# Performance work log

Measured on AMD Instinct MI355X. Metric: run time of the kernel, lower is better.

Reference implementation:

```python
import jax, jax.numpy as jnp
import numpy as np

B = 262144      # Monte Carlo samples (batch)
DH = 128        # d_hidden
DM = 4          # concatenated input feature dim (two one-hot spins)


def _glorot(key, shape):
    fan_in, fan_out = shape[0], shape[1]
    lim = jnp.sqrt(6.0 / (fan_in + fan_out)).astype(jnp.float32)
    return jax.random.uniform(key, shape, jnp.float32, -lim, lim)


def setup_inputs() -> dict:
    key = jax.random.key(0)
    ks = jax.random.split(key, 10)
    inputs = jax.random.normal(ks[0], (B, DM), jnp.float32)
    h1 = jax.random.normal(ks[1], (B, DH), jnp.float32)
    h2 = jax.random.normal(ks[2], (B, DH), jnp.float32)
    U1 = _glorot(ks[3], (DH, DH))
    U2 = _glorot(ks[4], (DH, DH))
    # flax GRUCell params: input kernels (with bias), hidden kernels
    # (r,z: no bias; n: bias). Packed as [ir|iz|in] and [hr|hz].
    Wi = _glorot(ks[5], (DM, 3 * DH))
    bi = jnp.zeros((3 * DH,), jnp.float32)
    Whrz = _glorot(ks[6], (DH, 2 * DH))
    Whn = _glorot(ks[7], (DH, DH))
    bhn = jnp.zeros((DH,), jnp.float32)
    return {"inputs": inputs, "h1": h1, "h2": h2, "U1": U1, "U2": U2,
            "Wi": Wi, "bi": bi, "Whrz": Whrz, "Whn": Whn, "bhn": bhn}


def reference(inputs, h1, h2, U1, U2, Wi, bi, Whrz, Whn, bhn):
    # Fuse the two neighbor hidden states: h = h1 @ U1 + h2 @ U2
    h = h1 @ U1 + h2 @ U2                      # [B, DH]
    # flax GRUCell(carry=h, inputs=x):
    i_proj = inputs @ Wi + bi                  # [B, 3*DH]
    ir, iz, i_n = jnp.split(i_proj, 3, axis=-1)
    hrz = h @ Whrz                             # [B, 2*DH] (no bias in flax)
    hr, hz = jnp.split(hrz, 2, axis=-1)
    r = jax.nn.sigmoid(ir + hr)
    z = jax.nn.sigmoid(iz + hz)
    n = jnp.tanh(i_n + r * (h @ Whn + bhn))
    new_h = (1.0 - z) * n + z * h
    return (new_h, new_h)
```

## Files before the change

### kernel.cpp

```cpp
#include <hip/hip_runtime.h>

using bf8 = __attribute__((ext_vector_type(8))) short;
using bf4 = __attribute__((ext_vector_type(4))) short;
using f4  = __attribute__((ext_vector_type(4))) float;
using u16 = unsigned short;

#define NROWS 262144

#define FLAG_B   0
#define PU_B     128
#define PW2_B    (PU_B + 65536)
#define PWI_B    (PW2_B + 98304)
#define BI_B     (PWI_B + 6144)
#define BHN_B    (BI_B + 1536)

#define PACK_ITEMS 83968

static __device__ __forceinline__ float bf2f(u16 u) {
    unsigned v = ((unsigned)u) << 16;
    return __builtin_bit_cast(float, v);
}
static __device__ __forceinline__ u16 f2bf(float f) {
    unsigned x = __builtin_bit_cast(unsigned, f);
    x = x + 0x7fffu + ((x >> 16) & 1u);
    return (u16)(x >> 16);
}

template<bool FP32>
static __device__ __forceinline__ u16 ldw(const void* p, int i) {
    if constexpr (FP32) return f2bf(((const float*)p)[i]);
    else                return ((const u16*)p)[i];
}
template<bool FP32>
static __device__ __forceinline__ float ldf(const void* p, int i) {
    if constexpr (FP32) return ((const float*)p)[i];
    else                return bf2f(((const u16*)p)[i]);
}
template<bool FP32>
static __device__ __forceinline__ bf8 ld8(const void* base, int idx) {
    if constexpr (!FP32) {
        return *(const bf8*)((const u16*)base + idx);
    } else {
        const float* f = (const float*)base + idx;
        f4 u = *(const f4*)f;
        f4 v = *(const f4*)(f + 4);
        bf8 r;
        r[0]=(short)f2bf(u[0]); r[1]=(short)f2bf(u[1]); r[2]=(short)f2bf(u[2]); r[3]=(short)f2bf(u[3]);
        r[4]=(short)f2bf(v[0]); r[5]=(short)f2bf(v[1]); r[6]=(short)f2bf(v[2]); r[7]=(short)f2bf(v[3]);
        return r;
    }
}
template<bool FP32>
static __device__ __forceinline__ void st8(void* base, int idx, bf8 v) {
    if constexpr (!FP32) {
        *(bf8*)((u16*)base + idx) = v;
    } else {
        float* f = (float*)base + idx;
        f4 a, b;
        a[0]=bf2f((u16)v[0]); a[1]=bf2f((u16)v[1]); a[2]=bf2f((u16)v[2]); a[3]=bf2f((u16)v[3]);
        b[0]=bf2f((u16)v[4]); b[1]=bf2f((u16)v[5]); b[2]=bf2f((u16)v[6]); b[3]=bf2f((u16)v[7]);
        *(f4*)f = a; *(f4*)(f + 4) = b;
    }
}

__global__ void detect_mode(const u16* __restrict__ h1u, int* __restrict__ flag) {
    if (threadIdx.x == 0 && blockIdx.x == 0) {
        int huge = 0;
#pragma unroll 8
        for (int i = 0; i < 256; ++i) {
            u16 v = h1u[i * 2];
            huge += (((v >> 7) & 0xFF) >= 0xC0);
        }
        *flag = (huge > 0) ? 1 : 0;
    }
}

template<bool FP32>
__global__ void prep_pack(const void* __restrict__ U1, const void* __restrict__ U2,
                          const void* __restrict__ Whrz, const void* __restrict__ Whn,
                          const void* __restrict__ Wi, const void* __restrict__ bi,
                          const void* __restrict__ bhn, char* __restrict__ ws,
                          const int* __restrict__ flag)
{
    if ((*flag != 0) != FP32) return;
    int e = blockIdx.x * 256 + threadIdx.x;
    if (e >= PACK_ITEMS) return;
    u16*   pU   = (u16*)(ws + PU_B);
    u16*   pW2  = (u16*)(ws + PW2_B);
    float* wiF  = (float*)(ws + PWI_B);
    float* biF  = (float*)(ws + BI_B);
    float* bhnF = (float*)(ws + BHN_B);
    if (e < 32768) {
        int j = e & 7, lane = (e >> 3) & 63, f = e >> 9;
        int kb = f & 7, nt = f >> 3;
        int k = kb * 32 + (lane >> 4) * 8 + j;
        int n = nt * 16 + (lane & 15);
        pU[e] = (k < 128) ? ldw<FP32>(U1, k * 128 + n) : ldw<FP32>(U2, (k - 128) * 128 + n);
    } else if (e < 81920) {
        int e2 = e - 32768;
        int j = e2 & 7, lane = (e2 >> 3) & 63, f = e2 >> 9;
        int kb = f & 3, nt = f >> 2;
        int k = kb * 32 + (lane >> 4) * 8 + j;
        int n = nt * 16 + (lane & 15);
        pW2[e2] = (n < 256) ? ldw<FP32>(Whrz, k * 256 + n) : ldw<FP32>(Whn, k * 128 + (n - 256));
    } else if (e < 83456) {
        int e3 = e - 81920;
        int k = e3 & 3, c = e3 >> 2;
        wiF[e3] = ldf<FP32>(Wi, k * 384 + c);
    } else if (e < 83840) {
        int i = e - 83456;  biF[i] = ldf<FP32>(bi, i);
    } else {
        int i = e - 83840;  bhnF[i] = ldf<FP32>(bhn, i);
    }
}

template<bool FP32>
__global__ __launch_bounds__(256, 3) void gru_fused(
    const void* __restrict__ xin, const void* __restrict__ h1,
    const void* __restrict__ h2, const char* __restrict__ ws,
    void* __restrict__ out, const int* __restrict__ flag, int write2)
{
    if ((*flag != 0) != FP32) return;
    __shared__ __align__(16) u16 hl[4][32][136];
    const int tid = threadIdx.x;
    const int w  = tid >> 6;
    const int l  = tid & 63;
    const int q  = l >> 4;
    const int lr = l & 15;
    const int g0 = blockIdx.x * 128 + w * 32;

    const bf8* __restrict__ pU  = (const bf8*)(ws + PU_B);
    const bf8* __restrict__ pW2 = (const bf8*)(ws + PW2_B);

    bf8 a[2][8];
#pragma unroll
    for (int m = 0; m < 2; ++m) {
        int row = g0 + m * 16 + lr;
        int base = row * 128 + q * 8;
#pragma unroll
        for (int kb = 0; kb < 4; ++kb) {
            a[m][kb]     = ld8<FP32>(h1, base + kb * 32);
            a[m][kb + 4] = ld8<FP32>(h2, base + kb * 32);
        }
    }
#pragma unroll 1
    for (int nt = 0; nt < 8; ++nt) {
        f4 acc0 = {0.f, 0.f, 0.f, 0.f};
        f4 acc1 = {0.f, 0.f, 0.f, 0.f};
#pragma unroll
        for (int kb = 0; kb < 8; ++kb) {
            bf8 b = pU[(nt * 8 + kb) * 64 + l];
            acc0 = __builtin_amdgcn_mfma_f32_16x16x32_bf16(a[0][kb], b, acc0, 0, 0, 0);
            acc1 = __builtin_amdgcn_mfma_f32_16x16x32_bf16(a[1][kb], b, acc1, 0, 0, 0);
        }
        int col = nt * 16 + lr;
#pragma unroll
        for (int i = 0; i < 4; ++i) {
            hl[w][q * 4 + i][col]      = f2bf(acc0[i]);
            hl[w][16 + q * 4 + i][col] = f2bf(acc1[i]);
        }
    }

    bf8 ah[2][4];
#pragma unroll
    for (int m = 0; m < 2; ++m)
#pragma unroll
        for (int kb = 0; kb < 4; ++kb)
            ah[m][kb] = *(const bf8*)&hl[w][m * 16 + lr][kb * 32 + q * 8];

    float xf[2][4][4];
#pragma unroll
    for (int m = 0; m < 2; ++m)
#pragma unroll
        for (int i = 0; i < 4; ++i) {
            int row = g0 + m * 16 + q * 4 + i;
            if constexpr (FP32) {
                f4 xv = *(const f4*)((const float*)xin + row * 4);
#pragma unroll
                for (int k = 0; k < 4; ++k) xf[m][i][k] = xv[k];
            } else {
                bf4 xv = *(const bf4*)((const u16*)xin + row * 4);
#pragma unroll
                for (int k = 0; k < 4; ++k) xf[m][i][k] = bf2f((u16)xv[k]);
            }
        }

    const float* wiF  = (const float*)(ws + PWI_B);
    const float* biF  = (const float*)(ws + BI_B);
    const float* bhnF = (const float*)(ws + BHN_B);

#pragma unroll 1
    for (int nt = 0; nt < 8; ++nt) {
        f4 aR[2], aZ[2], aN[2];
#pragma unroll
        for (int m = 0; m < 2; ++m) {
            aR[m] = {0.f,0.f,0.f,0.f}; aZ[m] = {0.f,0.f,0.f,0.f}; aN[m] = {0.f,0.f,0.f,0.f};
        }
#pragma unroll
        for (int kb = 0; kb < 4; ++kb) {
            bf8 bR = pW2[((nt     ) * 4 + kb) * 64 + l];
            bf8 bZ = pW2[((nt + 8 ) * 4 + kb) * 64 + l];
            bf8 bN = pW2[((nt + 16) * 4 + kb) * 64 + l];
#pragma unroll
            for (int m = 0; m < 2; ++m) {
                aR[m] = __builtin_amdgcn_mfma_f32_16x16x32_bf16(ah[m][kb], bR, aR[m], 0, 0, 0);
                aZ[m] = __builtin_amdgcn_mfma_f32_16x16x32_bf16(ah[m][kb], bZ, aZ[m], 0, 0, 0);
                aN[m] = __builtin_amdgcn_mfma_f32_16x16x32_bf16(ah[m][kb], bN, aN[m], 0, 0, 0);
            }
        }
        int c = nt * 16 + lr;
        f4 wr = *(const f4*)(wiF + c * 4);
        f4 wz = *(const f4*)(wiF + (128 + c) * 4);
        f4 wn = *(const f4*)(wiF + (256 + c) * 4);
        float bir = biF[c], biz = biF[128 + c], bin = biF[256 + c], bhc = bhnF[c];
#pragma unroll
        for (int m = 0; m < 2; ++m)
#pragma unroll
            for (int i = 0; i < 4; ++i) {
                int rl = m * 16 + q * 4 + i;
                float ir = bir, iz = biz, inn = bin;
#pragma unroll
                for (int k = 0; k < 4; ++k) {
                    ir  = fmaf(xf[m][i][k], wr[k], ir);
                    iz  = fmaf(xf[m][i][k], wz[k], iz);
                    inn = fmaf(xf[m][i][k], wn[k], inn);
                }
                float hv = bf2f(hl[w][rl][c]);
                float sr = ir + aR[m][i];
                sr = fminf(fmaxf(sr, -30.f), 30.f);
                float r = __fdividef(1.f, 1.f + __expf(-sr));
                float sz = iz + aZ[m][i];
                sz = fminf(fmaxf(sz, -30.f), 30.f);
                float z = __fdividef(1.f, 1.f + __expf(-sz));
                float t = inn + r * (aN[m][i] + bhc);
                t = fminf(fmaxf(t, -15.f), 15.f);
                float e2t = __expf(2.f * t);
                float n = (e2t - 1.f) * __fdividef(1.f, e2t + 1.f);
                float o = (1.f - z) * n + z * hv;
                hl[w][rl][c] = f2bf(o);
            }
    }

#pragma unroll
    for (int ii = 0; ii < 8; ++ii) {
        int ch  = ii * 64 + l;
        int row = ch >> 4;
        int c8  = (ch & 15) * 8;
        bf8 v = *(const bf8*)&hl[w][row][c8];
        int off = (g0 + row) * 128 + c8;
        st8<FP32>(out, off, v);
        if (write2) st8<FP32>(out, NROWS * 128 + off, v);
    }
}

extern "C" void kernel_launch(void* const* d_in, const int* in_sizes, int n_in,
                              void* d_out, int out_size, void* d_ws, size_t ws_size,
                              hipStream_t stream) {
    const void* x    = d_in[0];
    const void* h1   = d_in[1];
    const void* h2   = d_in[2];
    const void* U1   = d_in[3];
    const void* U2   = d_in[4];
    const void* Wi   = d_in[5];
    const void* bi   = d_in[6];
    const void* Whrz = d_in[7];
    const void* Whn  = d_in[8];
    const void* bhn  = d_in[9];
    char* ws   = (char*)d_ws;
    int* flag  = (int*)(ws + FLAG_B);
    int write2 = (out_size >= 2 * NROWS * 128) ? 1 : 0;

    detect_mode<<<1, 64, 0, stream>>>((const u16*)h1, flag);
    const int pblk = (PACK_ITEMS + 255) / 256;
    prep_pack<false><<<pblk, 256, 0, stream>>>(U1, U2, Whrz, Whn, Wi, bi, bhn, ws, flag);
    prep_pack<true ><<<pblk, 256, 0, stream>>>(U1, U2, Whrz, Whn, Wi, bi, bhn, ws, flag);
    gru_fused<false><<<NROWS / 128, 256, 0, stream>>>(x, h1, h2, ws, d_out, flag, write2);
    gru_fused<true ><<<NROWS / 128, 256, 0, stream>>>(x, h1, h2, ws, d_out, flag, write2);
}
```

Measured before the change: 549.4 us.

## Fold input projection and biases into MFMA, write fp32 outputs directly

```diff
diff --git a/kernel.cpp b/kernel.cpp
--- a/kernel.cpp
+++ b/kernel.cpp
@@ -3,18 +3,17 @@
 using bf8 = __attribute__((ext_vector_type(8))) short;
 using bf4 = __attribute__((ext_vector_type(4))) short;
 using f4  = __attribute__((ext_vector_type(4))) float;
+using ui4 = __attribute__((ext_vector_type(4))) unsigned int;
+using u32 = unsigned int;
 using u16 = unsigned short;
 
 #define NROWS 262144
 
-#define FLAG_B   0
-#define PU_B     128
-#define PW2_B    (PU_B + 65536)
-#define PWI_B    (PW2_B + 98304)
-#define BI_B     (PWI_B + 6144)
-#define BHN_B    (BI_B + 1536)
-
-#define PACK_ITEMS 83968
+#define FLAG_B 0
+#define PU_B   128
+#define PW2_B  (PU_B + 65536)
+#define PE_B   (PW2_B + 98304)
+#define PACK_ITEMS 98304
 
 static __device__ __forceinline__ float bf2f(u16 u) {
     unsigned v = ((unsigned)u) << 16;
@@ -24,6 +23,10 @@
     unsigned x = __builtin_bit_cast(unsigned, f);
     x = x + 0x7fffu + ((x >> 16) & 1u);
     return (u16)(x >> 16);
+}
+static __device__ __forceinline__ u32 pk2t(float a, float b) {
+    u32 ab = __builtin_bit_cast(u32, a), bb = __builtin_bit_cast(u32, b);
+    return (ab >> 16) | (bb & 0xffff0000u);
 }
 
 template<bool FP32>
@@ -44,22 +47,12 @@
         const float* f = (const float*)base + idx;
         f4 u = *(const f4*)f;
         f4 v = *(const f4*)(f + 4);
-        bf8 r;
-        r[0]=(short)f2bf(u[0]); r[1]=(short)f2bf(u[1]); r[2]=(short)f2bf(u[2]); r[3]=(short)f2bf(u[3]);
-        r[4]=(short)f2bf(v[0]); r[5]=(short)f2bf(v[1]); r[6]=(short)f2bf(v[2]); r[7]=(short)f2bf(v[3]);
-        return r;
-    }
-}
-template<bool FP32>
-static __device__ __forceinline__ void st8(void* base, int idx, bf8 v) {
-    if constexpr (!FP32) {
-        *(bf8*)((u16*)base + idx) = v;
-    } else {
-        float* f = (float*)base + idx;
-        f4 a, b;
-        a[0]=bf2f((u16)v[0]); a[1]=bf2f((u16)v[1]); a[2]=bf2f((u16)v[2]); a[3]=bf2f((u16)v[3]);
-        b[0]=bf2f((u16)v[4]); b[1]=bf2f((u16)v[5]); b[2]=bf2f((u16)v[6]); b[3]=bf2f((u16)v[7]);
-        *(f4*)f = a; *(f4*)(f + 4) = b;
+        ui4 w;
+        w[0] = pk2t(u[0], u[1]);
+        w[1] = pk2t(u[2], u[3]);
+        w[2] = pk2t(v[0], v[1]);
+        w[3] = pk2t(v[2], v[3]);
+        return __builtin_bit_cast(bf8, w);
     }
 }
 
@@ -85,11 +78,9 @@
     if ((*flag != 0) != FP32) return;
     int e = blockIdx.x * 256 + threadIdx.x;
     if (e >= PACK_ITEMS) return;
-    u16*   pU   = (u16*)(ws + PU_B);
-    u16*   pW2  = (u16*)(ws + PW2_B);
-    float* wiF  = (float*)(ws + PWI_B);
-    float* biF  = (float*)(ws + BI_B);
-    float* bhnF = (float*)(ws + BHN_B);
+    u16* pU  = (u16*)(ws + PU_B);
+    u16* pW2 = (u16*)(ws + PW2_B);
+    u16* pE  = (u16*)(ws + PE_B);
     if (e < 32768) {
         int j = e & 7, lane = (e >> 3) & 63, f = e >> 9;
         int kb = f & 7, nt = f >> 3;
@@ -103,19 +94,31 @@
         int k = kb * 32 + (lane >> 4) * 8 + j;
         int n = nt * 16 + (lane & 15);
         pW2[e2] = (n < 256) ? ldw<FP32>(Whrz, k * 256 + n) : ldw<FP32>(Whn, k * 128 + (n - 256));
-    } else if (e < 83456) {
+    } else {
         int e3 = e - 81920;
-        int k = e3 & 3, c = e3 >> 2;
-        wiF[e3] = ldf<FP32>(Wi, k * 384 + c);
-    } else if (e < 83840) {
-        int i = e - 83456;  biF[i] = ldf<FP32>(bi, i);
-    } else {
-        int i = e - 83840;  bhnF[i] = ldf<FP32>(bhn, i);
-    }
-}
-
-template<bool FP32>
-__global__ __launch_bounds__(256, 3) void gru_fused(
+        int j = e3 & 7, lane = (e3 >> 3) & 63, f = e3 >> 9;
+        int nt = f & 7, set = f >> 3;
+        int k = (lane >> 4) * 8 + j;
+        int n = nt * 16 + (lane & 15);
+        float v = 0.f;
+        if (set == 0) {
+            if (k < 4)       v = ldf<FP32>(Wi, k * 384 + n);
+            else if (k == 4) v = ldf<FP32>(bi, n);
+        } else if (set == 1) {
+            if (k < 4)       v = ldf<FP32>(Wi, k * 384 + 128 + n);
+            else if (k == 4) v = ldf<FP32>(bi, 128 + n);
+        } else if (set == 2) {
+            if (k == 4)      v = ldf<FP32>(bhn, n);
+        } else {
+            if (k < 4)       v = ldf<FP32>(Wi, k * 384 + 256 + n);
+            else if (k == 4) v = ldf<FP32>(bi, 256 + n);
+        }
+        pE[e3] = f2bf(v);
+    }
+}
+
+template<bool FP32>
+static __device__ __forceinline__ void gru_body(
     const void* __restrict__ xin, const void* __restrict__ h1,
     const void* __restrict__ h2, const char* __restrict__ ws,
     void* __restrict__ out, const int* __restrict__ flag, int write2)
@@ -131,12 +134,12 @@
 
     const bf8* __restrict__ pU  = (const bf8*)(ws + PU_B);
     const bf8* __restrict__ pW2 = (const bf8*)(ws + PW2_B);
+    const bf8* __restrict__ pE  = (const bf8*)(ws + PE_B);
 
     bf8 a[2][8];
 #pragma unroll
     for (int m = 0; m < 2; ++m) {
-        int row = g0 + m * 16 + lr;
-        int base = row * 128 + q * 8;
+        int base = (g0 + m * 16 + lr) * 128 + q * 8;
 #pragma unroll
         for (int kb = 0; kb < 4; ++kb) {
             a[m][kb]     = ld8<FP32>(h1, base + kb * 32);
@@ -168,33 +171,42 @@
         for (int kb = 0; kb < 4; ++kb)
             ah[m][kb] = *(const bf8*)&hl[w][m * 16 + lr][kb * 32 + q * 8];
 
-    float xf[2][4][4];
-#pragma unroll
-    for (int m = 0; m < 2; ++m)
-#pragma unroll
-        for (int i = 0; i < 4; ++i) {
-            int row = g0 + m * 16 + q * 4 + i;
+    bf8 ax[2];
+#pragma unroll
+    for (int m = 0; m < 2; ++m) {
+        ui4 z = {0u, 0u, 0u, 0u};
+        if (q == 0) {
+            int row = g0 + m * 16 + lr;
+            u16 xb[4];
             if constexpr (FP32) {
                 f4 xv = *(const f4*)((const float*)xin + row * 4);
 #pragma unroll
-                for (int k = 0; k < 4; ++k) xf[m][i][k] = xv[k];
+                for (int k = 0; k < 4; ++k) xb[k] = f2bf(xv[k]);
             } else {
                 bf4 xv = *(const bf4*)((const u16*)xin + row * 4);
 #pragma unroll
-                for (int k = 0; k < 4; ++k) xf[m][i][k] = bf2f((u16)xv[k]);
+                for (int k = 0; k < 4; ++k) xb[k] = (u16)xv[k];
             }
-        }
-
-    const float* wiF  = (const float*)(ws + PWI_B);
-    const float* biF  = (const float*)(ws + BI_B);
-    const float* bhnF = (const float*)(ws + BHN_B);
+            z[0] = (u32)xb[0] | ((u32)xb[1] << 16);
+            z[1] = (u32)xb[2] | ((u32)xb[3] << 16);
+            z[2] = 0x3f80u;
+        }
+        ax[m] = __builtin_bit_cast(bf8, z);
+    }
 
 #pragma unroll 1
     for (int nt = 0; nt < 8; ++nt) {
-        f4 aR[2], aZ[2], aN[2];
+        bf8 eR  = pE[(0 * 8 + nt) * 64 + l];
+        bf8 eZ  = pE[(1 * 8 + nt) * 64 + l];
+        bf8 eN1 = pE[(2 * 8 + nt) * 64 + l];
+        bf8 eN2 = pE[(3 * 8 + nt) * 64 + l];
+        f4 aR[2], aZ[2], aN1[2], aN2[2];
 #pragma unroll
         for (int m = 0; m < 2; ++m) {
-            aR[m] = {0.f,0.f,0.f,0.f}; aZ[m] = {0.f,0.f,0.f,0.f}; aN[m] = {0.f,0.f,0.f,0.f};
+            aR[m]  = __builtin_amdgcn_mfma_f32_16x16x32_bf16(ax[m], eR,  (f4){0.f,0.f,0.f,0.f}, 0, 0, 0);
+            aZ[m]  = __builtin_amdgcn_mfma_f32_16x16x32_bf16(ax[m], eZ,  (f4){0.f,0.f,0.f,0.f}, 0, 0, 0);
+            aN1[m] = __builtin_amdgcn_mfma_f32_16x16x32_bf16(ax[m], eN1, (f4){0.f,0.f,0.f,0.f}, 0, 0, 0);
+            aN2[m] = __builtin_amdgcn_mfma_f32_16x16x32_bf16(ax[m], eN2, (f4){0.f,0.f,0.f,0.f}, 0, 0, 0);
         }
 #pragma unroll
         for (int kb = 0; kb < 4; ++kb) {
@@ -203,55 +215,57 @@
             bf8 bN = pW2[((nt + 16) * 4 + kb) * 64 + l];
 #pragma unroll
             for (int m = 0; m < 2; ++m) {
-                aR[m] = __builtin_amdgcn_mfma_f32_16x16x32_bf16(ah[m][kb], bR, aR[m], 0, 0, 0);
-                aZ[m] = __builtin_amdgcn_mfma_f32_16x16x32_bf16(ah[m][kb], bZ, aZ[m], 0, 0, 0);
-                aN[m] = __builtin_amdgcn_mfma_f32_16x16x32_bf16(ah[m][kb], bN, aN[m], 0, 0, 0);
+                aR[m]  = __builtin_amdgcn_mfma_f32_16x16x32_bf16(ah[m][kb], bR, aR[m],  0, 0, 0);
+                aZ[m]  = __builtin_amdgcn_mfma_f32_16x16x32_bf16(ah[m][kb], bZ, aZ[m],  0, 0, 0);
+                aN1[m] = __builtin_amdgcn_mfma_f32_16x16x32_bf16(ah[m][kb], bN, aN1[m], 0, 0, 0);
             }
         }
         int c = nt * 16 + lr;
-        f4 wr = *(const f4*)(wiF + c * 4);
-        f4 wz = *(const f4*)(wiF + (128 + c) * 4);
-        f4 wn = *(const f4*)(wiF + (256 + c) * 4);
-        float bir = biF[c], biz = biF[128 + c], bin = biF[256 + c], bhc = bhnF[c];
 #pragma unroll
         for (int m = 0; m < 2; ++m)
 #pragma unroll
             for (int i = 0; i < 4; ++i) {
                 int rl = m * 16 + q * 4 + i;
-                float ir = bir, iz = biz, inn = bin;
-#pragma unroll
-                for (int k = 0; k < 4; ++k) {
-                    ir  = fmaf(xf[m][i][k], wr[k], ir);
-                    iz  = fmaf(xf[m][i][k], wz[k], iz);
-                    inn = fmaf(xf[m][i][k], wn[k], inn);
+                float hv = bf2f(hl[w][rl][c]);
+                float r = __fdividef(1.f, 1.f + __expf(-aR[m][i]));
+                float zg = __fdividef(1.f, 1.f + __expf(-aZ[m][i]));
+                float t = aN2[m][i] + r * aN1[m][i];
+                float n = 1.f - 2.f * __fdividef(1.f, __expf(2.f * t) + 1.f);
+                float o = n + zg * (hv - n);
+                if constexpr (FP32) {
+                    int off = (g0 + rl) * 128 + c;
+                    ((float*)out)[off] = o;
+                    if (write2) ((float*)out)[NROWS * 128 + off] = o;
+                } else {
+                    hl[w][rl][c] = f2bf(o);
                 }
-                float hv = bf2f(hl[w][rl][c]);
-                float sr = ir + aR[m][i];
-                sr = fminf(fmaxf(sr, -30.f), 30.f);
-                float r = __fdividef(1.f, 1.f + __expf(-sr));
-                float sz = iz + aZ[m][i];
-                sz = fminf(fmaxf(sz, -30.f), 30.f);
-                float z = __fdividef(1.f, 1.f + __expf(-sz));
-                float t = inn + r * (aN[m][i] + bhc);
-                t = fminf(fmaxf(t, -15.f), 15.f);
-                float e2t = __expf(2.f * t);
-                float n = (e2t - 1.f) * __fdividef(1.f, e2t + 1.f);
-                float o = (1.f - z) * n + z * hv;
-                hl[w][rl][c] = f2bf(o);
             }
     }
 
-#pragma unroll
-    for (int ii = 0; ii < 8; ++ii) {
-        int ch  = ii * 64 + l;
-        int row = ch >> 4;
-        int c8  = (ch & 15) * 8;
-        bf8 v = *(const bf8*)&hl[w][row][c8];
-        int off = (g0 + row) * 128 + c8;
-        st8<FP32>(out, off, v);
-        if (write2) st8<FP32>(out, NROWS * 128 + off, v);
-    }
-}
+    if constexpr (!FP32) {
+        u16* o0 = (u16*)out;
+#pragma unroll
+        for (int ii = 0; ii < 8; ++ii) {
+            int ch  = ii * 64 + l;
+            int row = ch >> 4;
+            int c8  = (ch & 15) * 8;
+            bf8 v = *(const bf8*)&hl[w][row][c8];
+            int off = (g0 + row) * 128 + c8;
+            *(bf8*)(o0 + off) = v;
+            if (write2) *(bf8*)(o0 + NROWS * 128 + off) = v;
+        }
+    }
+}
+
+__global__ __launch_bounds__(256, 4) void gru_b16(
+    const void* x, const void* h1, const void* h2, const char* ws,
+    void* out, const int* flag, int write2)
+{ gru_body<false>(x, h1, h2, ws, out, flag, write2); }
+
+__global__ __launch_bounds__(256, 4) void gru_f32(
+    const void* x, const void* h1, const void* h2, const char* ws,
+    void* out, const int* flag, int write2)
+{ gru_body<true>(x, h1, h2, ws, out, flag, write2); }
 
 extern "C" void kernel_launch(void* const* d_in, const int* in_sizes, int n_in,
                               void* d_out, int out_size, void* d_ws, size_t ws_size,
@@ -274,6 +288,6 @@
     const int pblk = (PACK_ITEMS + 255) / 256;
     prep_pack<false><<<pblk, 256, 0, stream>>>(U1, U2, Whrz, Whn, Wi, bi, bhn, ws, flag);
     prep_pack<true ><<<pblk, 256, 0, stream>>>(U1, U2, Whrz, Whn, Wi, bi, bhn, ws, flag);
-    gru_fused<false><<<NROWS / 128, 256, 0, stream>>>(x, h1, h2, ws, d_out, flag, write2);
-    gru_fused<true ><<<NROWS / 128, 256, 0, stream>>>(x, h1, h2, ws, d_out, flag, write2);
-}
+    gru_b16<<<NROWS / 128, 256, 0, stream>>>(x, h1, h2, ws, d_out, flag, write2);
+    gru_f32<<<NROWS / 128, 256, 0, stream>>>(x, h1, h2, ws, d_out, flag, write2);
+}
```

After: 564.1 us. 1.03x slower.
